# Kernel optimization log

Measured on AMD Instinct MI355X. Metric: run time of the kernel, lower is better.

Reference implementation:

```python
import jax, jax.numpy as jnp
import numpy as np

S, B, E, H, V, O = 1024, 256, 128, 256, 32000, 2


def setup_inputs() -> dict:
    key = jax.random.key(0)
    ks = jax.random.split(key, 6)
    inp = jax.random.randint(ks[0], (S, B), 0, V)                     # [S, B] time-major token ids
    lengths = jax.random.randint(ks[1], (B,), 1, S + 1)               # valid lengths in [1, S]
    emb_table = jax.random.normal(ks[2], (V, E), jnp.float32) * 0.1   # nn.Embedding weight
    w_ih = jax.random.normal(ks[3], (4 * H, E), jnp.float32) * 0.05   # LSTM weight_ih_l0 (gate order i,f,g,o)
    w_hh = jax.random.normal(ks[4], (4 * H, H), jnp.float32) * 0.05   # LSTM weight_hh_l0
    b_ih = jnp.zeros((4 * H,), jnp.float32)
    b_hh = jnp.zeros((4 * H,), jnp.float32)
    dec_w = jax.random.normal(ks[5], (O, H), jnp.float32) * 0.05      # decoder Linear (bias=False)
    h0 = jnp.zeros((1, B, H), jnp.float32)
    c0 = jnp.zeros((1, B, H), jnp.float32)
    return dict(inp=inp, lengths=lengths, h0=h0, c0=c0, emb_table=emb_table,
                w_ih=w_ih, w_hh=w_hh, b_ih=b_ih, b_hh=b_hh, dec_w=dec_w)


def reference(inp, lengths, h0, c0, emb_table, w_ih, w_hh, b_ih, b_hh, dec_w):
    emb = emb_table[inp]  # [S, B, E]
    bias = b_ih + b_hh

    def step(carry, x_t):
        h, c = carry
        gates = x_t @ w_ih.T + h @ w_hh.T + bias          # [B, 4H]
        i, f, g, o = jnp.split(gates, 4, axis=-1)         # pytorch gate order i,f,g,o
        i, f, o = jax.nn.sigmoid(i), jax.nn.sigmoid(f), jax.nn.sigmoid(o)
        g = jnp.tanh(g)
        c = f * c + i * g
        h = o * jnp.tanh(c)
        return (h, c), (h, c)

    _, (hs, cs) = jax.lax.scan(step, (h0[0], c0[0]), emb)  # hs, cs: [S, B, H]
    idx = lengths - 1
    b_arange = jnp.arange(B)
    last_h = hs[idx, b_arange]                             # [B, H] output at last valid step
    last_c = cs[idx, b_arange]
    decoded = jax.nn.sigmoid(last_h @ dec_w.T)             # [B, O]
    # packed-RNN final hidden = state at each sequence's own last valid step
    return decoded, (last_h[None], last_c[None])
```

## Files before the change

kernel.cpp:

```cpp
#include <hip/hip_runtime.h>
#include <hip/hip_bf16.h>
#include <hip/hip_fp16.h>

#define S_LEN 1024
#define BATCH 256
#define EDIM  128
#define HDIM  256
#define ODIM  2

typedef unsigned int uint32;
typedef unsigned long long uint64;
typedef _Float16 half_t;
typedef half_t half2v __attribute__((ext_vector_type(2)));
typedef half_t half8  __attribute__((ext_vector_type(8)));
typedef float  f32x4  __attribute__((ext_vector_type(4)));

#define OFF_WHHF   0
#define OFF_WIHF   131072
#define OFF_HBUF   196608
#define HBUF_DW    131072

__device__ __forceinline__ float sigf(float x)     { return 1.0f / (1.0f + __expf(-x)); }
__device__ __forceinline__ float tanhfast(float x) { return 1.0f - 2.0f / (__expf(2.0f * x) + 1.0f); }

__device__ __forceinline__ uint32 packh2(float a, float b) {
  union { uint32 u; half2v h; } c; c.h[0] = (half_t)a; c.h[1] = (half_t)b; return c.u;
}
__device__ __forceinline__ half8 as_h8(uint4 v) {
  union { uint4 u; half8 h; } c; c.u = v; return c.h;
}

#define MFMA16(A, B, C) __builtin_amdgcn_mfma_f32_16x16x32_f16(as_h8(A), as_h8(B), (C), 0, 0, 0)

__global__ void prep_kernel(const float* __restrict__ w_ih, const float* __restrict__ w_hh,
                            uint32* __restrict__ ws_u) {
  int id = blockIdx.x * 256 + threadIdx.x;
  if (id < 131072) {
    int q = id >> 15, T = (id >> 11) & 15, t = (id >> 8) & 7, l = (id >> 2) & 63, d = id & 3;
    int grow = (T >> 2) * 256 + q * 64 + (T & 3) * 16 + (l & 15);
    int k = t * 32 + (l >> 4) * 8 + 2 * d;
    ws_u[OFF_WHHF + id] = packh2(w_hh[grow * HDIM + k], w_hh[grow * HDIM + k + 1]);
  } else if (id < 131072 + 65536) {
    int i2 = id - 131072;
    int q = i2 >> 14, T = (i2 >> 10) & 15, t = (i2 >> 8) & 3, l = (i2 >> 2) & 63, d = i2 & 3;
    int grow = (T >> 2) * 256 + q * 64 + (T & 3) * 16 + (l & 15);
    int k = t * 32 + (l >> 4) * 8 + 2 * d;
    ws_u[OFF_WIHF + i2] = packh2(w_ih[grow * EDIM + k], w_ih[grow * EDIM + k + 1]);
  } else if (id < 131072 + 65536 + HBUF_DW) {
    ws_u[OFF_HBUF + (id - 131072 - 65536)] = 0;
  }
}

__global__ __launch_bounds__(256, 1) __attribute__((amdgpu_waves_per_eu(1)))
void lstm_kernel(
    const int* __restrict__ inp, const int* __restrict__ lengths,
    const float* __restrict__ h0, const float* __restrict__ c0,
    const float* __restrict__ emb,
    const float* __restrict__ b_ih, const float* __restrict__ b_hh,
    uint32* __restrict__ ws_u,
    float* __restrict__ outh, float* __restrict__ outc) {
  __shared__ uint32 x_l[2 * 16 * 68];
  __shared__ uint32 h_l[16 * 132];
  __shared__ int fast_sh;

  const int tid  = threadIdx.x;
  const int lane = tid & 63, w = tid >> 6;
  const int c = blockIdx.x & 15, q = blockIdx.x >> 4;
  const int n = lane & 15, p = lane >> 4;
  const int sb = tid >> 4, j = tid & 15;

  uint64* hb = (uint64*)(ws_u + OFF_HBUF);

  {
    uint32 xcc;
    asm volatile("s_getreg_b32 %0, hwreg(HW_REG_XCC_ID)" : "=s"(xcc));
    if (tid == 0) {
      int* sl = (int*)(ws_u + OFF_HBUF);
      const int sbase = (16 + c) * 4096;
      __hip_atomic_store(sl + sbase + 64 * q, (int)xcc + 1,
                         __ATOMIC_RELAXED, __HIP_MEMORY_SCOPE_AGENT);
      int ok = 1;
      for (int qq = 0; qq < 4; ++qq) {
        if (qq == q) continue;
        int v;
        do {
          v = __hip_atomic_load(sl + sbase + 64 * qq,
                                __ATOMIC_RELAXED, __HIP_MEMORY_SCOPE_AGENT);
        } while (v == 0);
        ok &= (v == (int)xcc + 1);
      }
      fast_sh = ok;
    }
  }

  int perm[8];
  perm[0] = 2 * q; perm[1] = 2 * q + 1;
#pragma unroll
  for (int i = 2; i < 8; ++i) {
    int base = i - 2;
    perm[i] = base < 2 * q ? base : base + 2;
  }
  int haddr[8];
#pragma unroll
  for (int i = 0; i < 8; ++i) haddr[i] = n * 132 + perm[i] * 16 + p * 4;

  const uint4* whhf = (const uint4*)(ws_u + OFF_WHHF);
  const uint4* wihf = (const uint4*)(ws_u + OFF_WIHF);
#define DECLW(g) uint4 ahh_##g##_0, ahh_##g##_1, ahh_##g##_2, ahh_##g##_3, \
                       ahh_##g##_4, ahh_##g##_5, ahh_##g##_6, ahh_##g##_7, \
                       aih_##g##_0, aih_##g##_1, aih_##g##_2, aih_##g##_3;
  DECLW(0) DECLW(1) DECLW(2) DECLW(3)
#define LOADW(g) { const int Tg = q * 16 + (g * 4 + w);                 \
    ahh_##g##_0 = whhf[(Tg * 8 + perm[0]) * 64 + lane];                 \
    ahh_##g##_1 = whhf[(Tg * 8 + perm[1]) * 64 + lane];                 \
    ahh_##g##_2 = whhf[(Tg * 8 + perm[2]) * 64 + lane];                 \
    ahh_##g##_3 = whhf[(Tg * 8 + perm[3]) * 64 + lane];                 \
    ahh_##g##_4 = whhf[(Tg * 8 + perm[4]) * 64 + lane];                 \
    ahh_##g##_5 = whhf[(Tg * 8 + perm[5]) * 64 + lane];                 \
    ahh_##g##_6 = whhf[(Tg * 8 + perm[6]) * 64 + lane];                 \
    ahh_##g##_7 = whhf[(Tg * 8 + perm[7]) * 64 + lane];                 \
    aih_##g##_0 = wihf[(Tg * 4 + 0) * 64 + lane];                       \
    aih_##g##_1 = wihf[(Tg * 4 + 1) * 64 + lane];                       \
    aih_##g##_2 = wihf[(Tg * 4 + 2) * 64 + lane];                       \
    aih_##g##_3 = wihf[(Tg * 4 + 3) * 64 + lane]; }
  LOADW(0) LOADW(1) LOADW(2) LOADW(3)

  const int ub  = 16 * w + 4 * p;
  const int col = 16 * c + n;
  const int len = lengths[col] - 1;
  float bias_[4][4], cst[4];
#pragma unroll
  for (int g = 0; g < 4; ++g) {
    float4 bi = *(const float4*)(b_ih + g * 256 + q * 64 + ub);
    float4 bh = *(const float4*)(b_hh + g * 256 + q * 64 + ub);
    bias_[g][0] = bi.x + bh.x; bias_[g][1] = bi.y + bh.y;
    bias_[g][2] = bi.z + bh.z; bias_[g][3] = bi.w + bh.w;
  }
  {
    float4 cv = *(const float4*)(c0 + col * HDIM + q * 64 + ub);
    cst[0] = cv.x; cst[1] = cv.y; cst[2] = cv.z; cst[3] = cv.w;
  }

  {
    const float4* hsrc = (const float4*)(h0 + (16 * c + sb) * HDIM) + 4 * j;
    float4 a0 = hsrc[0], a1 = hsrc[1], a2 = hsrc[2], a3 = hsrc[3];
    uint4 pk0 = { packh2(a0.x,a0.y), packh2(a0.z,a0.w), packh2(a1.x,a1.y), packh2(a1.z,a1.w) };
    uint4 pk1 = { packh2(a2.x,a2.y), packh2(a2.z,a2.w), packh2(a3.x,a3.y), packh2(a3.z,a3.w) };
    *(uint4*)(h_l + sb * 132 + 8 * j)     = pk0;
    *(uint4*)(h_l + sb * 132 + 8 * j + 4) = pk1;
    int tok = inp[16 * c + sb];
    const float4* xsrc = (const float4*)(emb + tok * EDIM) + 2 * j;
    float4 v0 = xsrc[0], v1 = xsrc[1];
    uint4 px = { packh2(v0.x,v0.y), packh2(v0.z,v0.w), packh2(v1.x,v1.y), packh2(v1.z,v1.w) };
    *(uint4*)(x_l + sb * 68 + 4 * j) = px;
  }
  __syncthreads();
  const bool fast = (fast_sh != 0);

  int ch[6];
#pragma unroll
  for (int i = 0; i < 6; ++i) {
    int idx6 = j * 6 + i;
    ch[i] = idx6 < q * 32 ? idx6 : idx6 + 32;
  }

  for (int s = 0; s < S_LEN; ++s) {
    const int par = s & 1;

    uint64 hv6[6] = {0, 0, 0, 0, 0, 0};
    const uint64* rp = hb + (((par ^ 1) * 16 + c) * 16 + sb) * 128;
    const uint64 *r0 = rp + ch[0], *r1 = rp + ch[1], *r2 = rp + ch[2],
                 *r3 = rp + ch[3], *r4 = rp + ch[4], *r5 = rp + ch[5];
    if (s > 0) {
      hv6[0] = __hip_atomic_load(r0, __ATOMIC_RELAXED, __HIP_MEMORY_SCOPE_AGENT);
      hv6[1] = __hip_atomic_load(r1, __ATOMIC_RELAXED, __HIP_MEMORY_SCOPE_AGENT);
      hv6[2] = __hip_atomic_load(r2, __ATOMIC_RELAXED, __HIP_MEMORY_SCOPE_AGENT);
      hv6[3] = __hip_atomic_load(r3, __ATOMIC_RELAXED, __HIP_MEMORY_SCOPE_AGENT);
      hv6[4] = __hip_atomic_load(r4, __ATOMIC_RELAXED, __HIP_MEMORY_SCOPE_AGENT);
      hv6[5] = __hip_atomic_load(r5, __ATOMIC_RELAXED, __HIP_MEMORY_SCOPE_AGENT);
    }
    int tok_next = 0;
    if (s + 1 < S_LEN) tok_next = inp[(s + 1) * BATCH + 16 * c + sb];

    f32x4 acc0 = { bias_[0][0], bias_[0][1], bias_[0][2], bias_[0][3] };
    f32x4 acc1 = { bias_[1][0], bias_[1][1], bias_[1][2], bias_[1][3] };
    f32x4 acc2 = { bias_[2][0], bias_[2][1], bias_[2][2], bias_[2][3] };
    f32x4 acc3 = { bias_[3][0], bias_[3][1], bias_[3][2], bias_[3][3] };
#define XMF(t) { uint4 xb = *(const uint4*)(x_l + par * 1088 + n * 68 + t * 16 + p * 4); \
    acc0 = MFMA16(aih_0_##t, xb, acc0); acc1 = MFMA16(aih_1_##t, xb, acc1);              \
    acc2 = MFMA16(aih_2_##t, xb, acc2); acc3 = MFMA16(aih_3_##t, xb, acc3); }
    XMF(0) XMF(1) XMF(2) XMF(3)
#define HMF(i) { uint4 hbv = *(const uint4*)(h_l + haddr[i]);                            \
    acc0 = MFMA16(ahh_0_##i, hbv, acc0); acc1 = MFMA16(ahh_1_##i, hbv, acc1);            \
    acc2 = MFMA16(ahh_2_##i, hbv, acc2); acc3 = MFMA16(ahh_3_##i, hbv, acc3); }
    HMF(0) HMF(1)

    if (s > 0) {
      const uint32 us = (uint32)s;
      while (!(((uint32)(hv6[0] >> 32) >= us) & ((uint32)(hv6[1] >> 32) >= us) &
               ((uint32)(hv6[2] >> 32) >= us) & ((uint32)(hv6[3] >> 32) >= us) &
               ((uint32)(hv6[4] >> 32) >= us) & ((uint32)(hv6[5] >> 32) >= us))) {
        hv6[0] = __hip_atomic_load(r0, __ATOMIC_RELAXED, __HIP_MEMORY_SCOPE_AGENT);
        hv6[1] = __hip_atomic_load(r1, __ATOMIC_RELAXED, __HIP_MEMORY_SCOPE_AGENT);
        hv6[2] = __hip_atomic_load(r2, __ATOMIC_RELAXED, __HIP_MEMORY_SCOPE_AGENT);
        hv6[3] = __hip_atomic_load(r3, __ATOMIC_RELAXED, __HIP_MEMORY_SCOPE_AGENT);
        hv6[4] = __hip_atomic_load(r4, __ATOMIC_RELAXED, __HIP_MEMORY_SCOPE_AGENT);
        hv6[5] = __hip_atomic_load(r5, __ATOMIC_RELAXED, __HIP_MEMORY_SCOPE_AGENT);
      }
#pragma unroll
      for (int i = 0; i < 6; ++i) h_l[sb * 132 + ch[i]] = (uint32)hv6[i];
    }
    __syncthreads();

    float4 xv0 = {0.f,0.f,0.f,0.f}, xv1 = {0.f,0.f,0.f,0.f};
    if (s + 1 < S_LEN) {
      const float4* xsrc = (const float4*)(emb + tok_next * EDIM) + 2 * j;
      xv0 = xsrc[0]; xv1 = xsrc[1];
    }

    HMF(2) HMF(3) HMF(4) HMF(5) HMF(6) HMF(7)

    float hv4[4];
#pragma unroll
    for (int r = 0; r < 4; ++r) {
      float iv = sigf(acc0[r]), fv = sigf(acc1[r]);
      float gv = tanhfast(acc2[r]), ov = sigf(acc3[r]);
      float cn = fv * cst[r] + iv * gv;
      cst[r] = cn;
      hv4[r] = ov * tanhfast(cn);
    }

    if (s + 1 < S_LEN) {
      uint32 pay0 = packh2(hv4[0], hv4[1]), pay1 = packh2(hv4[2], hv4[3]);
      const uint32 su = (uint32)(s + 1);
      const int P = q * 32 + 8 * w + 2 * p;
      uint64* wp = hb + (((par * 16 + c) * 16 + n) * 128 + P);
      uint64 pv0 = (uint64)pay0 | (((uint64)su) << 32);
      uint64 pv1 = (uint64)pay1 | (((uint64)su) << 32);
      if (fast) {
        __hip_atomic_store(wp,     pv0, __ATOMIC_RELAXED, __HIP_MEMORY_SCOPE_WORKGROUP);
        __hip_atomic_store(wp + 1, pv1, __ATOMIC_RELAXED, __HIP_MEMORY_SCOPE_WORKGROUP);
      } else {
        __hip_atomic_store(wp,     pv0, __ATOMIC_RELAXED, __HIP_MEMORY_SCOPE_AGENT);
        __hip_atomic_store(wp + 1, pv1, __ATOMIC_RELAXED, __HIP_MEMORY_SCOPE_AGENT);
      }
      *(uint2*)(h_l + n * 132 + P) = (uint2){ pay0, pay1 };
      uint4 px = { packh2(xv0.x,xv0.y), packh2(xv0.z,xv0.w), packh2(xv1.x,xv1.y), packh2(xv1.z,xv1.w) };
      *(uint4*)(x_l + (par ^ 1) * 1088 + sb * 68 + 4 * j) = px;
    }
    if (s == len) {
      float4 ho = { hv4[0], hv4[1], hv4[2], hv4[3] };
      float4 co = { cst[0], cst[1], cst[2], cst[3] };
      *(float4*)(outh + col * HDIM + q * 64 + ub) = ho;
      *(float4*)(outc + col * HDIM + q * 64 + ub) = co;
    }
    __syncthreads();
  }
}

__global__ __launch_bounds__(64) void decode_kernel(const float* __restrict__ outh,
                                                    const float* __restrict__ dec_w,
                                                    float* __restrict__ dec) {
  int b = blockIdx.x, l = threadIdx.x;
  float p0 = 0.f, p1 = 0.f;
#pragma unroll
  for (int m = 0; m < HDIM / 64; ++m) {
    float h = outh[b * HDIM + l + 64 * m];
    p0 = fmaf(h, dec_w[l + 64 * m], p0);
    p1 = fmaf(h, dec_w[HDIM + l + 64 * m], p1);
  }
#pragma unroll
  for (int off = 32; off > 0; off >>= 1) {
    p0 += __shfl_down(p0, off);
    p1 += __shfl_down(p1, off);
  }
  if (l == 0) {
    dec[b * ODIM + 0] = sigf(p0);
    dec[b * ODIM + 1] = sigf(p1);
  }
}

extern "C" void kernel_launch(void* const* d_in, const int* in_sizes, int n_in,
                              void* d_out, int out_size, void* d_ws, size_t ws_size,
                              hipStream_t stream) {
  const int*   inp     = (const int*)d_in[0];
  const int*   lengths = (const int*)d_in[1];
  const float* h0      = (const float*)d_in[2];
  const float* c0      = (const float*)d_in[3];
  const float* emb     = (const float*)d_in[4];
  const float* w_ih    = (const float*)d_in[5];
  const float* w_hh    = (const float*)d_in[6];
  const float* b_ih    = (const float*)d_in[7];
  const float* b_hh    = (const float*)d_in[8];
  const float* dec_w   = (const float*)d_in[9];

  uint32* ws_u = (uint32*)d_ws;

  float* dec  = (float*)d_out;
  float* outh = dec + BATCH * ODIM;
  float* outc = outh + BATCH * HDIM;

  const int prep_total = 131072 + 65536 + HBUF_DW;
  prep_kernel<<<(prep_total + 255) / 256, 256, 0, stream>>>(w_ih, w_hh, ws_u);
  lstm_kernel<<<64, 256, 0, stream>>>(inp, lengths, h0, c0, emb, b_ih, b_hh,
                                      ws_u, outh, outc);
  decode_kernel<<<BATCH, 64, 0, stream>>>(outh, dec_w, dec);
}
```

Measured before the change: 2.549 ms.

## Split hidden dimension across 2 blocks of 512 threads instead of 4 of 256

Each batch chunk is now handled by 2 workgroups of 8 waves instead of 4 workgroups of 4 waves, each owning 128 hidden units. Less of h has to travel between blocks through global memory each step, and each block waits on one peer instead of three. In exchange each block runs more waves and issues more MFMAs per step. The launch bounds change from one wave per EU to 512 threads, which adds register pressure from the 48 weight fragments held per thread.

```diff
diff --git a/kernel.cpp b/kernel.cpp
--- a/kernel.cpp
+++ b/kernel.cpp
@@ -36,14 +36,14 @@
                             uint32* __restrict__ ws_u) {
   int id = blockIdx.x * 256 + threadIdx.x;
   if (id < 131072) {
-    int q = id >> 15, T = (id >> 11) & 15, t = (id >> 8) & 7, l = (id >> 2) & 63, d = id & 3;
-    int grow = (T >> 2) * 256 + q * 64 + (T & 3) * 16 + (l & 15);
+    int q = id >> 16, T = (id >> 11) & 31, t = (id >> 8) & 7, l = (id >> 2) & 63, d = id & 3;
+    int grow = (T >> 3) * 256 + q * 128 + (T & 7) * 16 + (l & 15);
     int k = t * 32 + (l >> 4) * 8 + 2 * d;
     ws_u[OFF_WHHF + id] = packh2(w_hh[grow * HDIM + k], w_hh[grow * HDIM + k + 1]);
   } else if (id < 131072 + 65536) {
     int i2 = id - 131072;
-    int q = i2 >> 14, T = (i2 >> 10) & 15, t = (i2 >> 8) & 3, l = (i2 >> 2) & 63, d = i2 & 3;
-    int grow = (T >> 2) * 256 + q * 64 + (T & 3) * 16 + (l & 15);
+    int q = i2 >> 15, T = (i2 >> 10) & 31, t = (i2 >> 8) & 3, l = (i2 >> 2) & 63, d = i2 & 3;
+    int grow = (T >> 3) * 256 + q * 128 + (T & 7) * 16 + (l & 15);
     int k = t * 32 + (l >> 4) * 8 + 2 * d;
     ws_u[OFF_WIHF + i2] = packh2(w_ih[grow * EDIM + k], w_ih[grow * EDIM + k + 1]);
   } else if (id < 131072 + 65536 + HBUF_DW) {
@@ -51,8 +51,7 @@
   }
 }
 
-__global__ __launch_bounds__(256, 1) __attribute__((amdgpu_waves_per_eu(1)))
-void lstm_kernel(
+__global__ __launch_bounds__(512, 2) void lstm_kernel(
     const int* __restrict__ inp, const int* __restrict__ lengths,
     const float* __restrict__ h0, const float* __restrict__ c0,
     const float* __restrict__ emb,
@@ -67,7 +66,7 @@
   const int lane = tid & 63, w = tid >> 6;
   const int c = blockIdx.x & 15, q = blockIdx.x >> 4;
   const int n = lane & 15, p = lane >> 4;
-  const int sb = tid >> 4, j = tid & 15;
+  const int sb = tid >> 5, sk = tid & 31;
 
   uint64* hb = (uint64*)(ws_u + OFF_HBUF);
 
@@ -77,29 +76,21 @@
     if (tid == 0) {
       int* sl = (int*)(ws_u + OFF_HBUF);
       const int sbase = (16 + c) * 4096;
-      __hip_atomic_store(sl + sbase + 64 * q, (int)xcc + 1,
+      __hip_atomic_store(sl + sbase + 128 * q, (int)xcc + 1,
                          __ATOMIC_RELAXED, __HIP_MEMORY_SCOPE_AGENT);
-      int ok = 1;
-      for (int qq = 0; qq < 4; ++qq) {
-        if (qq == q) continue;
-        int v;
-        do {
-          v = __hip_atomic_load(sl + sbase + 64 * qq,
-                                __ATOMIC_RELAXED, __HIP_MEMORY_SCOPE_AGENT);
-        } while (v == 0);
-        ok &= (v == (int)xcc + 1);
-      }
-      fast_sh = ok;
+      int v;
+      do {
+        v = __hip_atomic_load(sl + sbase + 128 * (1 - q),
+                              __ATOMIC_RELAXED, __HIP_MEMORY_SCOPE_AGENT);
+      } while (v == 0);
+      fast_sh = (v == (int)xcc + 1);
     }
   }
 
   int perm[8];
-  perm[0] = 2 * q; perm[1] = 2 * q + 1;
-#pragma unroll
-  for (int i = 2; i < 8; ++i) {
-    int base = i - 2;
-    perm[i] = base < 2 * q ? base : base + 2;
-  }
+#pragma unroll
+  for (int i = 0; i < 8; ++i)
+    perm[i] = (i < 4) ? (4 * q + i) : (4 * (1 - q) + (i - 4));
   int haddr[8];
 #pragma unroll
   for (int i = 0; i < 8; ++i) haddr[i] = n * 132 + perm[i] * 16 + p * 4;
@@ -110,7 +101,7 @@
                        ahh_##g##_4, ahh_##g##_5, ahh_##g##_6, ahh_##g##_7, \
                        aih_##g##_0, aih_##g##_1, aih_##g##_2, aih_##g##_3;
   DECLW(0) DECLW(1) DECLW(2) DECLW(3)
-#define LOADW(g) { const int Tg = q * 16 + (g * 4 + w);                 \
+#define LOADW(g) { const int Tg = q * 32 + (g * 8 + w);                 \
     ahh_##g##_0 = whhf[(Tg * 8 + perm[0]) * 64 + lane];                 \
     ahh_##g##_1 = whhf[(Tg * 8 + perm[1]) * 64 + lane];                 \
     ahh_##g##_2 = whhf[(Tg * 8 + perm[2]) * 64 + lane];                 \
@@ -131,53 +122,39 @@
   float bias_[4][4], cst[4];
 #pragma unroll
   for (int g = 0; g < 4; ++g) {
-    float4 bi = *(const float4*)(b_ih + g * 256 + q * 64 + ub);
-    float4 bh = *(const float4*)(b_hh + g * 256 + q * 64 + ub);
+    float4 bi = *(const float4*)(b_ih + g * 256 + q * 128 + ub);
+    float4 bh = *(const float4*)(b_hh + g * 256 + q * 128 + ub);
     bias_[g][0] = bi.x + bh.x; bias_[g][1] = bi.y + bh.y;
     bias_[g][2] = bi.z + bh.z; bias_[g][3] = bi.w + bh.w;
   }
   {
-    float4 cv = *(const float4*)(c0 + col * HDIM + q * 64 + ub);
+    float4 cv = *(const float4*)(c0 + col * HDIM + q * 128 + ub);
     cst[0] = cv.x; cst[1] = cv.y; cst[2] = cv.z; cst[3] = cv.w;
   }
 
   {
-    const float4* hsrc = (const float4*)(h0 + (16 * c + sb) * HDIM) + 4 * j;
-    float4 a0 = hsrc[0], a1 = hsrc[1], a2 = hsrc[2], a3 = hsrc[3];
-    uint4 pk0 = { packh2(a0.x,a0.y), packh2(a0.z,a0.w), packh2(a1.x,a1.y), packh2(a1.z,a1.w) };
-    uint4 pk1 = { packh2(a2.x,a2.y), packh2(a2.z,a2.w), packh2(a3.x,a3.y), packh2(a3.z,a3.w) };
-    *(uint4*)(h_l + sb * 132 + 8 * j)     = pk0;
-    *(uint4*)(h_l + sb * 132 + 8 * j + 4) = pk1;
+    const float4* hsrc = (const float4*)(h0 + (16 * c + sb) * HDIM) + 2 * sk;
+    float4 a0 = hsrc[0], a1 = hsrc[1];
+    uint4 pk = { packh2(a0.x,a0.y), packh2(a0.z,a0.w), packh2(a1.x,a1.y), packh2(a1.z,a1.w) };
+    *(uint4*)(h_l + sb * 132 + 4 * sk) = pk;
     int tok = inp[16 * c + sb];
-    const float4* xsrc = (const float4*)(emb + tok * EDIM) + 2 * j;
-    float4 v0 = xsrc[0], v1 = xsrc[1];
-    uint4 px = { packh2(v0.x,v0.y), packh2(v0.z,v0.w), packh2(v1.x,v1.y), packh2(v1.z,v1.w) };
-    *(uint4*)(x_l + sb * 68 + 4 * j) = px;
+    float4 v = ((const float4*)(emb + tok * EDIM))[sk];
+    uint2 px = { packh2(v.x,v.y), packh2(v.z,v.w) };
+    *(uint2*)(x_l + sb * 68 + 2 * sk) = px;
   }
   __syncthreads();
   const bool fast = (fast_sh != 0);
 
-  int ch[6];
-#pragma unroll
-  for (int i = 0; i < 6; ++i) {
-    int idx6 = j * 6 + i;
-    ch[i] = idx6 < q * 32 ? idx6 : idx6 + 32;
-  }
+  const int ch0 = 64 * (1 - q) + 2 * sk;
 
   for (int s = 0; s < S_LEN; ++s) {
     const int par = s & 1;
 
-    uint64 hv6[6] = {0, 0, 0, 0, 0, 0};
+    uint64 hv0 = 0, hv1 = 0;
     const uint64* rp = hb + (((par ^ 1) * 16 + c) * 16 + sb) * 128;
-    const uint64 *r0 = rp + ch[0], *r1 = rp + ch[1], *r2 = rp + ch[2],
-                 *r3 = rp + ch[3], *r4 = rp + ch[4], *r5 = rp + ch[5];
     if (s > 0) {
-      hv6[0] = __hip_atomic_load(r0, __ATOMIC_RELAXED, __HIP_MEMORY_SCOPE_AGENT);
-      hv6[1] = __hip_atomic_load(r1, __ATOMIC_RELAXED, __HIP_MEMORY_SCOPE_AGENT);
-      hv6[2] = __hip_atomic_load(r2, __ATOMIC_RELAXED, __HIP_MEMORY_SCOPE_AGENT);
-      hv6[3] = __hip_atomic_load(r3, __ATOMIC_RELAXED, __HIP_MEMORY_SCOPE_AGENT);
-      hv6[4] = __hip_atomic_load(r4, __ATOMIC_RELAXED, __HIP_MEMORY_SCOPE_AGENT);
-      hv6[5] = __hip_atomic_load(r5, __ATOMIC_RELAXED, __HIP_MEMORY_SCOPE_AGENT);
+      hv0 = __hip_atomic_load(rp + ch0,     __ATOMIC_RELAXED, __HIP_MEMORY_SCOPE_AGENT);
+      hv1 = __hip_atomic_load(rp + ch0 + 1, __ATOMIC_RELAXED, __HIP_MEMORY_SCOPE_AGENT);
     }
     int tok_next = 0;
     if (s + 1 < S_LEN) tok_next = inp[(s + 1) * BATCH + 16 * c + sb];
@@ -193,32 +170,22 @@
 #define HMF(i) { uint4 hbv = *(const uint4*)(h_l + haddr[i]);                            \
     acc0 = MFMA16(ahh_0_##i, hbv, acc0); acc1 = MFMA16(ahh_1_##i, hbv, acc1);            \
     acc2 = MFMA16(ahh_2_##i, hbv, acc2); acc3 = MFMA16(ahh_3_##i, hbv, acc3); }
-    HMF(0) HMF(1)
+    HMF(0) HMF(1) HMF(2) HMF(3)
 
     if (s > 0) {
       const uint32 us = (uint32)s;
-      while (!(((uint32)(hv6[0] >> 32) >= us) & ((uint32)(hv6[1] >> 32) >= us) &
-               ((uint32)(hv6[2] >> 32) >= us) & ((uint32)(hv6[3] >> 32) >= us) &
-               ((uint32)(hv6[4] >> 32) >= us) & ((uint32)(hv6[5] >> 32) >= us))) {
-        hv6[0] = __hip_atomic_load(r0, __ATOMIC_RELAXED, __HIP_MEMORY_SCOPE_AGENT);
-        hv6[1] = __hip_atomic_load(r1, __ATOMIC_RELAXED, __HIP_MEMORY_SCOPE_AGENT);
-        hv6[2] = __hip_atomic_load(r2, __ATOMIC_RELAXED, __HIP_MEMORY_SCOPE_AGENT);
-        hv6[3] = __hip_atomic_load(r3, __ATOMIC_RELAXED, __HIP_MEMORY_SCOPE_AGENT);
-        hv6[4] = __hip_atomic_load(r4, __ATOMIC_RELAXED, __HIP_MEMORY_SCOPE_AGENT);
-        hv6[5] = __hip_atomic_load(r5, __ATOMIC_RELAXED, __HIP_MEMORY_SCOPE_AGENT);
+      while (!(((uint32)(hv0 >> 32) >= us) & ((uint32)(hv1 >> 32) >= us))) {
+        hv0 = __hip_atomic_load(rp + ch0,     __ATOMIC_RELAXED, __HIP_MEMORY_SCOPE_AGENT);
+        hv1 = __hip_atomic_load(rp + ch0 + 1, __ATOMIC_RELAXED, __HIP_MEMORY_SCOPE_AGENT);
       }
-#pragma unroll
-      for (int i = 0; i < 6; ++i) h_l[sb * 132 + ch[i]] = (uint32)hv6[i];
+      *(uint2*)(h_l + sb * 132 + ch0) = (uint2){ (uint32)hv0, (uint32)hv1 };
     }
     __syncthreads();
 
-    float4 xv0 = {0.f,0.f,0.f,0.f}, xv1 = {0.f,0.f,0.f,0.f};
-    if (s + 1 < S_LEN) {
-      const float4* xsrc = (const float4*)(emb + tok_next * EDIM) + 2 * j;
-      xv0 = xsrc[0]; xv1 = xsrc[1];
-    }
-
-    HMF(2) HMF(3) HMF(4) HMF(5) HMF(6) HMF(7)
+    float4 xv = {0.f, 0.f, 0.f, 0.f};
+    if (s + 1 < S_LEN) xv = ((const float4*)(emb + tok_next * EDIM))[sk];
+
+    HMF(4) HMF(5) HMF(6) HMF(7)
 
     float hv4[4];
 #pragma unroll
@@ -233,7 +200,7 @@
     if (s + 1 < S_LEN) {
       uint32 pay0 = packh2(hv4[0], hv4[1]), pay1 = packh2(hv4[2], hv4[3]);
       const uint32 su = (uint32)(s + 1);
-      const int P = q * 32 + 8 * w + 2 * p;
+      const int P = 64 * q + 8 * w + 2 * p;
       uint64* wp = hb + (((par * 16 + c) * 16 + n) * 128 + P);
       uint64 pv0 = (uint64)pay0 | (((uint64)su) << 32);
       uint64 pv1 = (uint64)pay1 | (((uint64)su) << 32);
@@ -245,14 +212,14 @@
         __hip_atomic_store(wp + 1, pv1, __ATOMIC_RELAXED, __HIP_MEMORY_SCOPE_AGENT);
       }
       *(uint2*)(h_l + n * 132 + P) = (uint2){ pay0, pay1 };
-      uint4 px = { packh2(xv0.x,xv0.y), packh2(xv0.z,xv0.w), packh2(xv1.x,xv1.y), packh2(xv1.z,xv1.w) };
-      *(uint4*)(x_l + (par ^ 1) * 1088 + sb * 68 + 4 * j) = px;
+      uint2 px = { packh2(xv.x, xv.y), packh2(xv.z, xv.w) };
+      *(uint2*)(x_l + (par ^ 1) * 1088 + sb * 68 + 2 * sk) = px;
     }
     if (s == len) {
       float4 ho = { hv4[0], hv4[1], hv4[2], hv4[3] };
       float4 co = { cst[0], cst[1], cst[2], cst[3] };
-      *(float4*)(outh + col * HDIM + q * 64 + ub) = ho;
-      *(float4*)(outc + col * HDIM + q * 64 + ub) = co;
+      *(float4*)(outh + col * HDIM + q * 128 + ub) = ho;
+      *(float4*)(outc + col * HDIM + q * 128 + ub) = co;
     }
     __syncthreads();
   }
@@ -302,7 +269,7 @@
 
   const int prep_total = 131072 + 65536 + HBUF_DW;
   prep_kernel<<<(prep_total + 255) / 256, 256, 0, stream>>>(w_ih, w_hh, ws_u);
-  lstm_kernel<<<64, 256, 0, stream>>>(inp, lengths, h0, c0, emb, b_ih, b_hh,
+  lstm_kernel<<<32, 512, 0, stream>>>(inp, lengths, h0, c0, emb, b_ih, b_hh,
                                       ws_u, outh, outc);
   decode_kernel<<<BATCH, 64, 0, stream>>>(outh, dec_w, dec);
 }
```

Measured after the change: 3.589 ms. 1.41x slower.
